# Optimization experiments

Hardware: AMD Instinct MI355X
Metric: run time of the kernel (lower is better)

## Reference

```python
import jax, jax.numpy as jnp
import numpy as np

NUM_HEADS = 8

def setup_inputs() -> dict:
    key = jax.random.key(0)
    ks = jax.random.split(key, 12)
    T, B, C, D = 2048, 4, 512, 512
    s = 1.0 / np.sqrt(C)
    return {
        "key_in": jax.random.normal(ks[0], (T, B, C), jnp.float32),
        "value_in": jax.random.normal(ks[1], (T, B, C), jnp.float32),
        "query_in": jax.random.normal(ks[2], (T, B, C), jnp.float32),
        "Wk": jax.random.normal(ks[3], (C, D), jnp.float32) * s,
        "bk": jax.random.normal(ks[4], (D,), jnp.float32) * 0.01,
        "Wv": jax.random.normal(ks[5], (C, D), jnp.float32) * s,
        "bv": jax.random.normal(ks[6], (D,), jnp.float32) * 0.01,
        "Wq": jax.random.normal(ks[7], (C, D), jnp.float32) * s,
        "bq": jax.random.normal(ks[8], (D,), jnp.float32) * 0.01,
        "Wo": jax.random.normal(ks[9], (D, D), jnp.float32) * (1.0 / np.sqrt(D)),
        "bo": jax.random.normal(ks[10], (D,), jnp.float32) * 0.01,
    }

def reference(key_in, value_in, query_in, Wk, bk, Wv, bv, Wq, bq, Wo, bo):
    T, B, C = query_in.shape
    D = Wq.shape[1]
    H = NUM_HEADS
    hd = D // H
    scale = 1.0 / np.sqrt(hd).astype(np.float32)
    # Linear projections on (T, B, C) -> (T, B, D), then the original's
    # row-major view(B, -1, H, hd) followed by transpose(1, 2) -> (B, H, T, hd)
    def proj(x, W, b):
        y = x @ W + b                      # (T, B, D)
        return y.reshape(B, -1, H, hd).transpose(0, 2, 1, 3)  # (B, H, T, hd)
    q = proj(query_in, Wq, bq)
    k = proj(key_in, Wk, bk)
    v = proj(value_in, Wv, bv)
    scores = jnp.einsum("bhqd,bhkd->bhqk", q, k) * scale  # (B, H, T, T)
    attn = jax.nn.softmax(scores, axis=-1)
    x = jnp.einsum("bhqk,bhkd->bhqd", attn, v)            # (B, H, T, hd)
    x = x.transpose(0, 2, 1, 3).reshape(T, B, D)          # matches .view(T, B, d_model)
    return x @ Wo + bo
```

## Files before the change

### kernel.cpp

```cpp
#include <hip/hip_runtime.h>
#include <math.h>

#define MROWS 8192
#define DM    512
#define SEQL  2048
#define HDIM  64

typedef __attribute__((ext_vector_type(4))) float floatx4;
typedef _Float16 half2v __attribute__((ext_vector_type(2)));
typedef _Float16 half4v __attribute__((ext_vector_type(4)));
typedef _Float16 half8v __attribute__((ext_vector_type(8)));

#define CEXP 0.18033688011f

__device__ __forceinline__ void gll16(const void* g, void* l) {
    __builtin_amdgcn_global_load_lds(
        (const __attribute__((address_space(1))) unsigned int*)g,
        (__attribute__((address_space(3))) unsigned int*)l, 16, 0, 0);
}

__device__ __forceinline__ half4v pack4(float a, float b, float c, float d) {
    half2v lo = __builtin_bit_cast(half2v, __builtin_amdgcn_cvt_pkrtz(a, b));
    half2v hi = __builtin_bit_cast(half2v, __builtin_amdgcn_cvt_pkrtz(c, d));
    half4v r;
    r[0] = lo[0]; r[1] = lo[1]; r[2] = hi[0]; r[3] = hi[1];
    return r;
}

__global__ __launch_bounds__(256) void transw(const float* __restrict__ w0,
                                              const float* __restrict__ w1,
                                              const float* __restrict__ w2,
                                              const float* __restrict__ w3,
                                              _Float16* __restrict__ t0,
                                              _Float16* __restrict__ t1,
                                              _Float16* __restrict__ t2,
                                              _Float16* __restrict__ t3) {
    __shared__ float tile[32][33];
    const float* W = blockIdx.z == 0 ? w0 : (blockIdx.z == 1 ? w1 : (blockIdx.z == 2 ? w2 : w3));
    _Float16* T = blockIdx.z == 0 ? t0 : (blockIdx.z == 1 ? t1 : (blockIdx.z == 2 ? t2 : t3));
    const float sc = (blockIdx.z == 0) ? CEXP : 1.0f;
    const int tx = threadIdx.x & 31, ty = threadIdx.x >> 5;
    const int x = blockIdx.x * 32 + tx;
    const int y0 = blockIdx.y * 32;
#pragma unroll
    for (int i = 0; i < 4; ++i)
        tile[ty + i * 8][tx] = W[(size_t)(y0 + ty + i * 8) * DM + x];
    __syncthreads();
    const int xo = y0 + tx;
#pragma unroll
    for (int i = 0; i < 4; ++i)
        T[(size_t)(blockIdx.x * 32 + ty + i * 8) * DM + xo] = (_Float16)(tile[tx][ty + i * 8] * sc);
}

__global__ __launch_bounds__(256, 3) void proj_gemm(
        const float* __restrict__ q32, const float* __restrict__ k32, const float* __restrict__ v32,
        const _Float16* __restrict__ Wq, const _Float16* __restrict__ Wk, const _Float16* __restrict__ Wv,
        const float* __restrict__ bq, const float* __restrict__ bk, const float* __restrict__ bv,
        _Float16* __restrict__ Qo, _Float16* __restrict__ Ko, _Float16* __restrict__ Vto) {
    __shared__ _Float16 As[128 * 64];
    __shared__ _Float16 Bs[128 * 64];
    const int z = blockIdx.z;
    const float* A32    = z == 0 ? q32 : (z == 1 ? k32 : v32);
    const _Float16* Bt  = z == 0 ? Wq : (z == 1 ? Wk : Wv);
    const float* bias   = z == 0 ? bq : (z == 1 ? bk : bv);
    const float bscale  = z == 0 ? CEXP : 1.0f;

    const int tid = threadIdx.x;
    const int w = tid >> 6, wr = w >> 1, wc = w & 1;
    const int l15 = tid & 15, quad = (tid & 63) >> 4;
    const int m0 = blockIdx.x * 128, n0 = blockIdx.y * 128;

    const int arow = tid >> 1, ah = tid & 1;
    const float* Asrc = &A32[(size_t)(m0 + arow) * DM + ah * 32];
    _Float16* Adst = &As[arow * 64];
    const int asw = arow & 7;

    floatx4 acc[4][4];
#pragma unroll
    for (int i = 0; i < 4; ++i)
#pragma unroll
        for (int j = 0; j < 4; ++j) acc[i][j] = (floatx4){0.f, 0.f, 0.f, 0.f};

    for (int kt = 0; kt < DM / 64; ++kt) {
        __syncthreads();
        floatx4 f[8];
        {
            const float* s = Asrc + (size_t)kt * 64;
#pragma unroll
            for (int q = 0; q < 8; ++q) f[q] = *(const floatx4*)&s[q * 4];
        }
#pragma unroll
        for (int i = 0; i < 4; ++i) {
            const int c = i * 256 + tid;
            const int row = c >> 3, g = c & 7;
            const int kg = g ^ (row & 7);
            gll16(&Bt[(size_t)(n0 + row) * DM + kt * 64 + kg * 8], &Bs[c * 8]);
        }
#pragma unroll
        for (int t = 0; t < 4; ++t) {
            half8v o;
            o[0] = (_Float16)f[2 * t][0]; o[1] = (_Float16)f[2 * t][1];
            o[2] = (_Float16)f[2 * t][2]; o[3] = (_Float16)f[2 * t][3];
            o[4] = (_Float16)f[2 * t + 1][0]; o[5] = (_Float16)f[2 * t + 1][1];
            o[6] = (_Float16)f[2 * t + 1][2]; o[7] = (_Float16)f[2 * t + 1][3];
            const int g = ah * 4 + t;
            *(half8v*)&Adst[(g ^ asw) * 8] = o;
        }
        __syncthreads();
#pragma unroll
        for (int ks = 0; ks < 2; ++ks) {
            half8v af[4], bf[4];
#pragma unroll
            for (int i = 0; i < 4; ++i) {
                const int row = wr * 64 + i * 16 + l15;
                af[i] = *(const half8v*)&As[row * 64 + (((ks * 4 + quad)) ^ (row & 7)) * 8];
            }
#pragma unroll
            for (int j = 0; j < 4; ++j) {
                const int row = wc * 64 + j * 16 + l15;
                bf[j] = *(const half8v*)&Bs[row * 64 + (((ks * 4 + quad)) ^ (row & 7)) * 8];
            }
#pragma unroll
            for (int i = 0; i < 4; ++i)
#pragma unroll
                for (int j = 0; j < 4; ++j)
                    acc[i][j] = __builtin_amdgcn_mfma_f32_16x16x32_f16(af[i], bf[j], acc[i][j], 0, 0, 0);
        }
    }
#pragma unroll
    for (int j = 0; j < 4; ++j) {
        const int col = n0 + wc * 64 + j * 16 + l15;
        const float bv4 = bias[col] * bscale;
#pragma unroll
        for (int i = 0; i < 4; ++i) {
            const int rb = m0 + wr * 64 + i * 16 + quad * 4;
            if (z == 2) {
                const int g = rb >> 11, seq = rb & 2047;
                half4v pv;
#pragma unroll
                for (int r = 0; r < 4; ++r) pv[r] = (_Float16)(acc[i][j][r] + bv4);
                *(half4v*)&Vto[((size_t)g * DM + col) * SEQL + seq] = pv;
            } else {
                _Float16* oh = z == 0 ? Qo : Ko;
#pragma unroll
                for (int r = 0; r < 4; ++r)
                    oh[(size_t)(rb + r) * DM + col] = (_Float16)(acc[i][j][r] + bv4);
            }
        }
    }
}

__global__ __launch_bounds__(256, 4) void out_gemm(
        const _Float16* __restrict__ O16,
        const _Float16* __restrict__ Wo, const float* __restrict__ bo,
        float* __restrict__ out) {
    __shared__ _Float16 Bs[256 * 64];
    __shared__ _Float16 As[32 * 64];
    const int tid = threadIdx.x;
    const int w = tid >> 6;
    const int l15 = tid & 15, quad = (tid & 63) >> 4;
    const int n0 = blockIdx.x * 256, m0 = blockIdx.y * 32;

    const int arow = tid >> 3, ag = tid & 7;
    const int akg = ag ^ (arow & 7);

    floatx4 acc[2][4];
#pragma unroll
    for (int i = 0; i < 2; ++i)
#pragma unroll
        for (int j = 0; j < 4; ++j) acc[i][j] = (floatx4){0.f, 0.f, 0.f, 0.f};

    for (int kt = 0; kt < DM / 64; ++kt) {
        __syncthreads();
#pragma unroll
        for (int i = 0; i < 8; ++i) {
            const int c = i * 256 + tid;
            const int row = c >> 3, g = c & 7;
            const int kg = g ^ (row & 7);
            gll16(&Wo[(size_t)(n0 + row) * DM + kt * 64 + kg * 8], &Bs[c * 8]);
        }
        gll16(&O16[(size_t)(m0 + arow) * DM + kt * 64 + akg * 8], &As[tid * 8]);
        __syncthreads();
#pragma unroll
        for (int ks = 0; ks < 2; ++ks) {
            half8v af[2], bfr[4];
#pragma unroll
            for (int i = 0; i < 2; ++i) {
                const int row = i * 16 + l15;
                af[i] = *(const half8v*)&As[row * 64 + ((ks * 4 + quad) ^ (row & 7)) * 8];
            }
#pragma unroll
            for (int j = 0; j < 4; ++j) {
                const int row = w * 64 + j * 16 + l15;
                bfr[j] = *(const half8v*)&Bs[row * 64 + ((ks * 4 + quad) ^ (row & 7)) * 8];
            }
#pragma unroll
            for (int i = 0; i < 2; ++i)
#pragma unroll
                for (int j = 0; j < 4; ++j)
                    acc[i][j] = __builtin_amdgcn_mfma_f32_16x16x32_f16(af[i], bfr[j], acc[i][j], 0, 0, 0);
        }
    }
#pragma unroll
    for (int j = 0; j < 4; ++j) {
        const int col = n0 + w * 64 + j * 16 + l15;
        const float bv4 = bo[col];
#pragma unroll
        for (int i = 0; i < 2; ++i) {
            const int rb = m0 + i * 16 + quad * 4;
#pragma unroll
            for (int r = 0; r < 4; ++r)
                out[(size_t)(rb + r) * DM + col] = acc[i][j][r] + bv4;
        }
    }
}

__global__ __launch_bounds__(256, 4) void attn_mfma(const _Float16* __restrict__ Q16,
                                                    const _Float16* __restrict__ K16,
                                                    const _Float16* __restrict__ Vt,
                                                    _Float16* __restrict__ O16) {
    __shared__ _Float16 Ks[2][64 * 64];
    __shared__ _Float16 Vs[2][64 * 64];

    const int tid  = threadIdx.x;
    const int lane = tid & 63;
    const int l15  = lane & 15;
    const int quad = lane >> 4;

    const int pair  = blockIdx.y;
    const int grp   = pair >> 3;
    const int h     = pair & 7;
    const int q0    = blockIdx.x * 128;
    const int rQ    = grp * SEQL + q0 + (tid >> 6) * 32;
    const int cb    = h * HDIM;
    const int NIT   = SEQL / 64;

    const _Float16* Kbase = K16 + (size_t)grp * SEQL * DM + cb;
    const _Float16* Vbase = Vt + (size_t)grp * DM * SEQL + (size_t)cb * SEQL;

    half8v qf[2][2];
#pragma unroll
    for (int qt = 0; qt < 2; ++qt)
#pragma unroll
        for (int ks = 0; ks < 2; ++ks)
            qf[qt][ks] = *(const half8v*)&Q16[(size_t)(rQ + qt * 16 + l15) * DM + cb + ks * 32 + quad * 8];

    floatx4 oacc[2][4], lacc[2];
#pragma unroll
    for (int qt = 0; qt < 2; ++qt) {
        lacc[qt] = (floatx4){0.f, 0.f, 0.f, 0.f};
#pragma unroll
        for (int dt = 0; dt < 4; ++dt) oacc[qt][dt] = (floatx4){0.f, 0.f, 0.f, 0.f};
    }
    half4v ones;
    ones[0] = (_Float16)1.f; ones[1] = (_Float16)1.f; ones[2] = (_Float16)1.f; ones[3] = (_Float16)1.f;

#define STAGE(KT, B)                                                            \
    {                                                                           \
        _Float16* ksb = &Ks[B][0];                                              \
        _Float16* vsb = &Vs[B][0];                                              \
        _Pragma("unroll")                                                       \
        for (int i_ = 0; i_ < 4; ++i_) {                                        \
            const int c_ = i_ * 256 + tid;                                      \
            if (c_ < 512) {                                                     \
                const int key_ = c_ >> 3, g_ = c_ & 7;                          \
                const int dg_ = g_ ^ (key_ & 7);                                \
                gll16(&Kbase[(size_t)((KT) * 64 + key_) * DM + dg_ * 8],        \
                      &ksb[c_ * 8]);                                            \
            } else {                                                            \
                const int cv_ = c_ - 512;                                       \
                const int d_ = cv_ >> 3, g_ = cv_ & 7;                          \
                const int kg_ = g_ ^ (d_ & 7);                                  \
                gll16(&Vbase[(size_t)d_ * SEQL + (KT) * 64 + kg_ * 8],          \
                      &vsb[cv_ * 8]);                                           \
            }                                                                   \
        }                                                                       \
    }

    STAGE(0, 0)

    for (int it = 0; it < NIT; ++it) {
        const int cur = it & 1;
        __syncthreads();
        if (it + 1 < NIT) STAGE(it + 1, cur ^ 1)

        const _Float16* ksb = &Ks[cur][0];
        const _Float16* vsb = &Vs[cur][0];

        floatx4 st[4][2];
#pragma unroll
        for (int ktile = 0; ktile < 4; ++ktile) {
            const int key = ktile * 16 + l15;
            const half8v kf0 = *(const half8v*)&ksb[key * 64 + ((0 + quad) ^ (key & 7)) * 8];
            const half8v kf1 = *(const half8v*)&ksb[key * 64 + ((4 + quad) ^ (key & 7)) * 8];
#pragma unroll
            for (int qt = 0; qt < 2; ++qt) {
                floatx4 z = {0.f, 0.f, 0.f, 0.f};
                z = __builtin_amdgcn_mfma_f32_16x16x32_f16(kf0, qf[qt][0], z, 0, 0, 0);
                st[ktile][qt] = __builtin_amdgcn_mfma_f32_16x16x32_f16(kf1, qf[qt][1], z, 0, 0, 0);
            }
        }

        half4v pa[4][2];
#pragma unroll
        for (int ktile = 0; ktile < 4; ++ktile)
#pragma unroll
            for (int qt = 0; qt < 2; ++qt)
                pa[ktile][qt] = pack4(__builtin_amdgcn_exp2f(st[ktile][qt][0]),
                                      __builtin_amdgcn_exp2f(st[ktile][qt][1]),
                                      __builtin_amdgcn_exp2f(st[ktile][qt][2]),
                                      __builtin_amdgcn_exp2f(st[ktile][qt][3]));

#pragma unroll
        for (int qt = 0; qt < 2; ++qt)
#pragma unroll
            for (int ktile = 0; ktile < 4; ++ktile)
                lacc[qt] = __builtin_amdgcn_mfma_f32_16x16x16f16(pa[ktile][qt], ones, lacc[qt], 0, 0, 0);

#pragma unroll
        for (int dt = 0; dt < 4; ++dt) {
            const int d = dt * 16 + l15;
#pragma unroll
            for (int ktile = 0; ktile < 4; ++ktile) {
                const int G = ktile * 2 + (quad >> 1);
                const int slot = G ^ (d & 7);
                const half4v vf = *(const half4v*)&vsb[d * 64 + slot * 8 + (quad & 1) * 4];
#pragma unroll
                for (int qt = 0; qt < 2; ++qt)
                    oacc[qt][dt] = __builtin_amdgcn_mfma_f32_16x16x16f16(pa[ktile][qt], vf, oacc[qt][dt], 0, 0, 0);
            }
        }
    }

#pragma unroll
    for (int qt = 0; qt < 2; ++qt)
#pragma unroll
        for (int r = 0; r < 4; ++r) {
            const int qrow = rQ + qt * 16 + quad * 4 + r;
            const size_t rowoff = (size_t)qrow * DM + cb;
            const float inv = 1.0f / lacc[qt][r];
#pragma unroll
            for (int dt = 0; dt < 4; ++dt)
                O16[rowoff + dt * 16 + l15] = (_Float16)(oacc[qt][dt][r] * inv);
        }
}

extern "C" void kernel_launch(void* const* d_in, const int* in_sizes, int n_in,
                              void* d_out, int out_size, void* d_ws, size_t ws_size,
                              hipStream_t stream) {
    const float* key_in   = (const float*)d_in[0];
    const float* value_in = (const float*)d_in[1];
    const float* query_in = (const float*)d_in[2];
    const float* Wk = (const float*)d_in[3];
    const float* bk = (const float*)d_in[4];
    const float* Wv = (const float*)d_in[5];
    const float* bv = (const float*)d_in[6];
    const float* Wq = (const float*)d_in[7];
    const float* bq = (const float*)d_in[8];
    const float* Wo = (const float*)d_in[9];
    const float* bo = (const float*)d_in[10];
    float* out = (float*)d_out;

    const size_t MAT = (size_t)MROWS * DM;
    _Float16* Q16  = (_Float16*)d_ws;
    _Float16* K16  = Q16 + MAT;
    _Float16* Vtb  = K16 + MAT;
    _Float16* Wqt  = Vtb + MAT;
    _Float16* Wkt  = Wqt + DM * DM;
    _Float16* Wvt  = Wkt + DM * DM;
    _Float16* Wot  = Wvt + DM * DM;
    _Float16* O16  = Wot + DM * DM;

    const dim3 blk(256);

    transw<<<dim3(16, 16, 4), blk, 0, stream>>>(Wq, Wk, Wv, Wo, Wqt, Wkt, Wvt, Wot);

    proj_gemm<<<dim3(MROWS / 128, DM / 128, 3), blk, 0, stream>>>(
        query_in, key_in, value_in, Wqt, Wkt, Wvt, bq, bk, bv, Q16, K16, Vtb);

    attn_mfma<<<dim3(SEQL / 128, 32), blk, 0, stream>>>(Q16, K16, Vtb, O16);

    out_gemm<<<dim3(2, MROWS / 32), blk, 0, stream>>>(O16, Wot, bo, out);
}
```

Baseline: 199.4 us.

## Retile output GEMM to 128x128 and halve attention query tile per block

The output projection GEMM moves from a 32x256 block tile to a 128x128 tile with a 2x2 warp layout, giving a more balanced A/B reuse and fewer blocks. The attention kernel now assigns 16 query rows per warp instead of 32, which doubles the grid and cuts per-thread register use. In exchange, each K/V tile loaded into LDS is reused by half as many queries, so K/V traffic per unit of work doubles.

```diff
diff --git a/kernel.cpp b/kernel.cpp
--- a/kernel.cpp
+++ b/kernel.cpp
@@ -150,64 +150,67 @@
     }
 }
 
-__global__ __launch_bounds__(256, 4) void out_gemm(
+__global__ __launch_bounds__(256, 3) void out_gemm(
         const _Float16* __restrict__ O16,
         const _Float16* __restrict__ Wo, const float* __restrict__ bo,
         float* __restrict__ out) {
-    __shared__ _Float16 Bs[256 * 64];
-    __shared__ _Float16 As[32 * 64];
+    __shared__ _Float16 As[128 * 64];
+    __shared__ _Float16 Bs[128 * 64];
     const int tid = threadIdx.x;
-    const int w = tid >> 6;
+    const int w = tid >> 6, wr = w >> 1, wc = w & 1;
     const int l15 = tid & 15, quad = (tid & 63) >> 4;
-    const int n0 = blockIdx.x * 256, m0 = blockIdx.y * 32;
-
-    const int arow = tid >> 3, ag = tid & 7;
-    const int akg = ag ^ (arow & 7);
-
-    floatx4 acc[2][4];
-#pragma unroll
-    for (int i = 0; i < 2; ++i)
+    const int m0 = blockIdx.x * 128, n0 = blockIdx.y * 128;
+
+    floatx4 acc[4][4];
+#pragma unroll
+    for (int i = 0; i < 4; ++i)
 #pragma unroll
         for (int j = 0; j < 4; ++j) acc[i][j] = (floatx4){0.f, 0.f, 0.f, 0.f};
 
     for (int kt = 0; kt < DM / 64; ++kt) {
         __syncthreads();
 #pragma unroll
-        for (int i = 0; i < 8; ++i) {
+        for (int i = 0; i < 4; ++i) {
+            const int c = i * 256 + tid;
+            const int row = c >> 3, g = c & 7;
+            const int kg = g ^ (row & 7);
+            gll16(&O16[(size_t)(m0 + row) * DM + kt * 64 + kg * 8], &As[c * 8]);
+        }
+#pragma unroll
+        for (int i = 0; i < 4; ++i) {
             const int c = i * 256 + tid;
             const int row = c >> 3, g = c & 7;
             const int kg = g ^ (row & 7);
             gll16(&Wo[(size_t)(n0 + row) * DM + kt * 64 + kg * 8], &Bs[c * 8]);
         }
-        gll16(&O16[(size_t)(m0 + arow) * DM + kt * 64 + akg * 8], &As[tid * 8]);
         __syncthreads();
 #pragma unroll
         for (int ks = 0; ks < 2; ++ks) {
-            half8v af[2], bfr[4];
-#pragma unroll
-            for (int i = 0; i < 2; ++i) {
-                const int row = i * 16 + l15;
+            half8v af[4], bf[4];
+#pragma unroll
+            for (int i = 0; i < 4; ++i) {
+                const int row = wr * 64 + i * 16 + l15;
                 af[i] = *(const half8v*)&As[row * 64 + ((ks * 4 + quad) ^ (row & 7)) * 8];
             }
 #pragma unroll
             for (int j = 0; j < 4; ++j) {
-                const int row = w * 64 + j * 16 + l15;
-                bfr[j] = *(const half8v*)&Bs[row * 64 + ((ks * 4 + quad) ^ (row & 7)) * 8];
-            }
-#pragma unroll
-            for (int i = 0; i < 2; ++i)
+                const int row = wc * 64 + j * 16 + l15;
+                bf[j] = *(const half8v*)&Bs[row * 64 + ((ks * 4 + quad) ^ (row & 7)) * 8];
+            }
+#pragma unroll
+            for (int i = 0; i < 4; ++i)
 #pragma unroll
                 for (int j = 0; j < 4; ++j)
-                    acc[i][j] = __builtin_amdgcn_mfma_f32_16x16x32_f16(af[i], bfr[j], acc[i][j], 0, 0, 0);
+                    acc[i][j] = __builtin_amdgcn_mfma_f32_16x16x32_f16(af[i], bf[j], acc[i][j], 0, 0, 0);
         }
     }
 #pragma unroll
     for (int j = 0; j < 4; ++j) {
-        const int col = n0 + w * 64 + j * 16 + l15;
+        const int col = n0 + wc * 64 + j * 16 + l15;
         const float bv4 = bo[col];
 #pragma unroll
-        for (int i = 0; i < 2; ++i) {
-            const int rb = m0 + i * 16 + quad * 4;
+        for (int i = 0; i < 4; ++i) {
+            const int rb = m0 + wr * 64 + i * 16 + quad * 4;
 #pragma unroll
             for (int r = 0; r < 4; ++r)
                 out[(size_t)(rb + r) * DM + col] = acc[i][j][r] + bv4;
@@ -230,28 +233,23 @@
     const int pair  = blockIdx.y;
     const int grp   = pair >> 3;
     const int h     = pair & 7;
-    const int q0    = blockIdx.x * 128;
-    const int rQ    = grp * SEQL + q0 + (tid >> 6) * 32;
+    const int q0    = blockIdx.x * 64;
+    const int rQ    = grp * SEQL + q0 + (tid >> 6) * 16;
     const int cb    = h * HDIM;
     const int NIT   = SEQL / 64;
 
     const _Float16* Kbase = K16 + (size_t)grp * SEQL * DM + cb;
     const _Float16* Vbase = Vt + (size_t)grp * DM * SEQL + (size_t)cb * SEQL;
 
-    half8v qf[2][2];
-#pragma unroll
-    for (int qt = 0; qt < 2; ++qt)
-#pragma unroll
-        for (int ks = 0; ks < 2; ++ks)
-            qf[qt][ks] = *(const half8v*)&Q16[(size_t)(rQ + qt * 16 + l15) * DM + cb + ks * 32 + quad * 8];
-
-    floatx4 oacc[2][4], lacc[2];
-#pragma unroll
-    for (int qt = 0; qt < 2; ++qt) {
-        lacc[qt] = (floatx4){0.f, 0.f, 0.f, 0.f};
-#pragma unroll
-        for (int dt = 0; dt < 4; ++dt) oacc[qt][dt] = (floatx4){0.f, 0.f, 0.f, 0.f};
-    }
+    half8v qf[2];
+#pragma unroll
+    for (int ks = 0; ks < 2; ++ks)
+        qf[ks] = *(const half8v*)&Q16[(size_t)(rQ + l15) * DM + cb + ks * 32 + quad * 8];
+
+    floatx4 oacc[4], lacc;
+    lacc = (floatx4){0.f, 0.f, 0.f, 0.f};
+#pragma unroll
+    for (int dt = 0; dt < 4; ++dt) oacc[dt] = (floatx4){0.f, 0.f, 0.f, 0.f};
     half4v ones;
     ones[0] = (_Float16)1.f; ones[1] = (_Float16)1.f; ones[2] = (_Float16)1.f; ones[3] = (_Float16)1.f;
 
@@ -287,35 +285,28 @@
         const _Float16* ksb = &Ks[cur][0];
         const _Float16* vsb = &Vs[cur][0];
 
-        floatx4 st[4][2];
+        floatx4 st[4];
 #pragma unroll
         for (int ktile = 0; ktile < 4; ++ktile) {
             const int key = ktile * 16 + l15;
             const half8v kf0 = *(const half8v*)&ksb[key * 64 + ((0 + quad) ^ (key & 7)) * 8];
             const half8v kf1 = *(const half8v*)&ksb[key * 64 + ((4 + quad) ^ (key & 7)) * 8];
-#pragma unroll
-            for (int qt = 0; qt < 2; ++qt) {
-                floatx4 z = {0.f, 0.f, 0.f, 0.f};
-                z = __builtin_amdgcn_mfma_f32_16x16x32_f16(kf0, qf[qt][0], z, 0, 0, 0);
-                st[ktile][qt] = __builtin_amdgcn_mfma_f32_16x16x32_f16(kf1, qf[qt][1], z, 0, 0, 0);
-            }
-        }
-
-        half4v pa[4][2];
+            floatx4 z = {0.f, 0.f, 0.f, 0.f};
+            z = __builtin_amdgcn_mfma_f32_16x16x32_f16(kf0, qf[0], z, 0, 0, 0);
+            st[ktile] = __builtin_amdgcn_mfma_f32_16x16x32_f16(kf1, qf[1], z, 0, 0, 0);
+        }
+
+        half4v pa[4];
 #pragma unroll
         for (int ktile = 0; ktile < 4; ++ktile)
-#pragma unroll
-            for (int qt = 0; qt < 2; ++qt)
-                pa[ktile][qt] = pack4(__builtin_amdgcn_exp2f(st[ktile][qt][0]),
-                                      __builtin_amdgcn_exp2f(st[ktile][qt][1]),
-                                      __builtin_amdgcn_exp2f(st[ktile][qt][2]),
-                                      __builtin_amdgcn_exp2f(st[ktile][qt][3]));
-
-#pragma unroll
-        for (int qt = 0; qt < 2; ++qt)
-#pragma unroll
-            for (int ktile = 0; ktile < 4; ++ktile)
-                lacc[qt] = __builtin_amdgcn_mfma_f32_16x16x16f16(pa[ktile][qt], ones, lacc[qt], 0, 0, 0);
+            pa[ktile] = pack4(__builtin_amdgcn_exp2f(st[ktile][0]),
+                              __builtin_amdgcn_exp2f(st[ktile][1]),
+                              __builtin_amdgcn_exp2f(st[ktile][2]),
+                              __builtin_amdgcn_exp2f(st[ktile][3]));
+
+#pragma unroll
+        for (int ktile = 0; ktile < 4; ++ktile)
+            lacc = __builtin_amdgcn_mfma_f32_16x16x16f16(pa[ktile], ones, lacc, 0, 0, 0);
 
 #pragma unroll
         for (int dt = 0; dt < 4; ++dt) {
@@ -325,24 +316,20 @@
                 const int G = ktile * 2 + (quad >> 1);
                 const int slot = G ^ (d & 7);
                 const half4v vf = *(const half4v*)&vsb[d * 64 + slot * 8 + (quad & 1) * 4];
-#pragma unroll
-                for (int qt = 0; qt < 2; ++qt)
-                    oacc[qt][dt] = __builtin_amdgcn_mfma_f32_16x16x16f16(pa[ktile][qt], vf, oacc[qt][dt], 0, 0, 0);
-            }
-        }
-    }
-
-#pragma unroll
-    for (int qt = 0; qt < 2; ++qt)
-#pragma unroll
-        for (int r = 0; r < 4; ++r) {
-            const int qrow = rQ + qt * 16 + quad * 4 + r;
-            const size_t rowoff = (size_t)qrow * DM + cb;
-            const float inv = 1.0f / lacc[qt][r];
-#pragma unroll
-            for (int dt = 0; dt < 4; ++dt)
-                O16[rowoff + dt * 16 + l15] = (_Float16)(oacc[qt][dt][r] * inv);
-        }
+                oacc[dt] = __builtin_amdgcn_mfma_f32_16x16x16f16(pa[ktile], vf, oacc[dt], 0, 0, 0);
+            }
+        }
+    }
+
+#pragma unroll
+    for (int r = 0; r < 4; ++r) {
+        const int qrow = rQ + quad * 4 + r;
+        const size_t rowoff = (size_t)qrow * DM + cb;
+        const float inv = 1.0f / lacc[r];
+#pragma unroll
+        for (int dt = 0; dt < 4; ++dt)
+            O16[rowoff + dt * 16 + l15] = (_Float16)(oacc[dt][r] * inv);
+    }
 }
 
 extern "C" void kernel_launch(void* const* d_in, const int* in_sizes, int n_in,
@@ -378,7 +365,7 @@
     proj_gemm<<<dim3(MROWS / 128, DM / 128, 3), blk, 0, stream>>>(
         query_in, key_in, value_in, Wqt, Wkt, Wvt, bq, bk, bv, Q16, K16, Vtb);
 
-    attn_mfma<<<dim3(SEQL / 128, 32), blk, 0, stream>>>(Q16, K16, Vtb, O16);
-
-    out_gemm<<<dim3(2, MROWS / 32), blk, 0, stream>>>(O16, Wot, bo, out);
-}
+    attn_mfma<<<dim3(SEQL / 64, 32), blk, 0, stream>>>(Q16, K16, Vtb, O16);
+
+    out_gemm<<<dim3(MROWS / 128, DM / 128), blk, 0, stream>>>(O16, Wot, bo, out);
+}
```

Result: slower. 209.7 us (+5.2%).
